# Kernel optimization log

Measured on AMD Instinct MI355X. Metric: run time of the kernel, lower is better.

## Reference

```python
import jax, jax.numpy as jnp
import numpy as np

NEG = -1e7  # matches replace_masked value -10000000.0


def tree_lstm(x, graph, wx, bx, uh, bh):
    # x: (B,T,I); graph: (B,T,T); wx: (4,H,I) gates [i,f,o,u]; uh: (4,H,H)
    B, T, _ = x.shape
    H = wx.shape[1]
    # precompute input projections for all gates/timesteps: (B,T,4,H)
    xg = jnp.einsum('bti,ghi->btgh', x, wx) + bx[None, None]
    h0 = jnp.zeros((B, T, H), x.dtype)

    def step(carry, j):
        h, c = carry
        h_j = h[:, j]  # still zeros at step j, as in the original code
        i = jax.nn.sigmoid(xg[:, j, 0] + h_j @ uh[0].T + bh[0])
        o = jax.nn.sigmoid(xg[:, j, 2] + h_j @ uh[2].T + bh[2])
        u = jnp.tanh(xg[:, j, 3] + h_j @ uh[3].T + bh[3])
        # forget gate against every node's hidden state: (B,T,H)
        f = jax.nn.sigmoid(xg[:, j, 1][:, None, :] + h @ uh[1].T + bh[1])
        # masked neighbor aggregation: bmm(mask, f*c) with mask row j
        c_j = i * u + jnp.einsum('bt,bth->bh', graph[:, j], f * c)
        h_j_new = o * jnp.tanh(c_j)
        return (h.at[:, j].set(h_j_new), c.at[:, j].set(c_j)), None

    (h, c), _ = jax.lax.scan(step, (h0, jnp.zeros_like(h0)), jnp.arange(T))
    return h, c


def masked_softmax(scores, key_mask):
    # scores: (B,Q,K); key_mask: (B,K)
    scores = jnp.where(key_mask[:, None, :] > 0, scores, NEG)
    return jax.nn.softmax(scores, axis=-1)


def pool(v, mask):
    avg = jnp.sum(v * mask[:, :, None], axis=1) / jnp.sum(mask, axis=1, keepdims=True)
    mx = jnp.max(jnp.where(mask[:, :, None] > 0, v, NEG), axis=1)
    return avg, mx


def esim_forward(premises, premises_lengths, hypotheses, hypotheses_lengths,
                 lgraph, rgraph, emb,
                 enc_wx, enc_bx, enc_uh, enc_bh,
                 comp_wx, comp_bx, comp_uh, comp_bh,
                 proj_w, proj_b, cls_w1, cls_b1, cls_w2, cls_b2):
    Tp = premises.shape[1]
    Th = hypotheses.shape[1]
    p_mask = (jnp.arange(Tp)[None, :] < premises_lengths[:, None]).astype(emb.dtype)
    h_mask = (jnp.arange(Th)[None, :] < hypotheses_lengths[:, None]).astype(emb.dtype)

    emb_p = emb[premises]
    emb_h = emb[hypotheses]

    enc_p, _ = tree_lstm(emb_p, lgraph, enc_wx, enc_bx, enc_uh, enc_bh)
    enc_h, _ = tree_lstm(emb_h, rgraph, enc_wx, enc_bx, enc_uh, enc_bh)

    # soft alignment attention
    sim = jnp.einsum('bph,bqh->bpq', enc_p, enc_h)
    att_p = masked_softmax(sim, h_mask) @ enc_h                      # (B,Tp,H)
    att_h = masked_softmax(sim.transpose(0, 2, 1), p_mask) @ enc_p   # (B,Th,H)

    enh_p = jnp.concatenate([enc_p, att_p, enc_p - att_p, enc_p * att_p], axis=-1)
    enh_h = jnp.concatenate([enc_h, att_h, enc_h - att_h, enc_h * att_h], axis=-1)

    proj_p = jax.nn.relu(enh_p @ proj_w.T + proj_b)
    proj_h = jax.nn.relu(enh_h @ proj_w.T + proj_b)

    v_ai, _ = tree_lstm(proj_p, lgraph, comp_wx, comp_bx, comp_uh, comp_bh)
    v_bj, _ = tree_lstm(proj_h, rgraph, comp_wx, comp_bx, comp_uh, comp_bh)

    a_avg, a_max = pool(v_ai, p_mask)
    b_avg, b_max = pool(v_bj, h_mask)
    v = jnp.concatenate([a_avg, a_max, b_avg, b_max], axis=1)

    hid = jnp.tanh(v @ cls_w1.T + cls_b1)
    logits = hid @ cls_w2.T + cls_b2
    return logits


def setup_inputs() -> dict:
    B, T, E, H, V, C = 32, 128, 300, 300, 50000, 3
    key = jax.random.key(0)
    ks = jax.random.split(key, 20)
    premises = jax.random.randint(ks[0], (B, T), 1, V)
    premises_lengths = jax.random.randint(ks[1], (B,), T // 2, T + 1)
    hypotheses = jax.random.randint(ks[2], (B, T), 1, V)
    hypotheses_lengths = jax.random.randint(ks[3], (B,), T // 2, T + 1)
    # sparse binary adjacency (~1-2 children per node), as in dependency trees
    lgraph = (jax.random.uniform(ks[4], (B, T, T)) < 0.01).astype(jnp.float32)
    rgraph = (jax.random.uniform(ks[5], (B, T, T)) < 0.01).astype(jnp.float32)
    emb = jax.random.normal(ks[6], (V, E), jnp.float32) * 0.05
    emb = emb.at[0].set(0.0)  # padding_idx=0

    def g(k, shape, fan_in):
        return jax.random.normal(k, shape, jnp.float32) * (1.0 / np.sqrt(fan_in))

    return {
        'premises': premises, 'premises_lengths': premises_lengths,
        'hypotheses': hypotheses, 'hypotheses_lengths': hypotheses_lengths,
        'lgraph': lgraph, 'rgraph': rgraph, 'emb': emb,
        'enc_wx': g(ks[7], (4, H, E), E), 'enc_bx': jnp.zeros((4, H), jnp.float32),
        'enc_uh': g(ks[8], (4, H, H), H), 'enc_bh': jnp.zeros((4, H), jnp.float32),
        'comp_wx': g(ks[9], (4, H, H), H), 'comp_bx': jnp.zeros((4, H), jnp.float32),
        'comp_uh': g(ks[10], (4, H, H), H), 'comp_bh': jnp.zeros((4, H), jnp.float32),
        'proj_w': g(ks[11], (H, 4 * H), 4 * H), 'proj_b': jnp.zeros((H,), jnp.float32),
        'cls_w1': g(ks[12], (H, 4 * H), 4 * H), 'cls_b1': jnp.zeros((H,), jnp.float32),
        'cls_w2': g(ks[13], (C, H), H), 'cls_b2': jnp.zeros((C,), jnp.float32),
    }


def reference(premises, premises_lengths, hypotheses, hypotheses_lengths,
              lgraph, rgraph, emb,
              enc_wx, enc_bx, enc_uh, enc_bh,
              comp_wx, comp_bx, comp_uh, comp_bh,
              proj_w, proj_b, cls_w1, cls_b1, cls_w2, cls_b2):
    return esim_forward(premises, premises_lengths, hypotheses, hypotheses_lengths,
                        lgraph, rgraph, emb,
                        enc_wx, enc_bx, enc_uh, enc_bh,
                        comp_wx, comp_bx, comp_uh, comp_bh,
                        proj_w, proj_b, cls_w1, cls_b1, cls_w2, cls_b2)
```

## Files before the change

kernel.cpp:

```cpp
#include <hip/hip_runtime.h>
#include <math.h>

#define B_ 32
#define T_ 128
#define H_ 300
#define HG 1200
#define LMAX 10
#define WLCAP 8192
#define ECAP 2048
#define NEGV -10000000.0f

typedef __attribute__((ext_vector_type(8))) short bf16x8;
typedef __attribute__((ext_vector_type(4))) float f32x4;
typedef unsigned short ushort_t;

__device__ __forceinline__ float sigm(float x){ return 1.f/(1.f+expf(-x)); }

__device__ __forceinline__ unsigned short f2bf(float x){
  union { float f; unsigned int u; } c; c.f = x;
  unsigned int u = c.u;
  return (unsigned short)((u + 0x7fffu + ((u >> 16) & 1u)) >> 16);
}
__device__ __forceinline__ float bf2f(unsigned short h){
  union { unsigned int u; float f; } c; c.u = ((unsigned int)h) << 16;
  return c.f;
}

__global__ __launch_bounds__(256) void k_prep_all(
    const float* __restrict__ enc_uh, const float* __restrict__ comp_uh,
    const float* __restrict__ enc_wx, const float* __restrict__ comp_wx,
    const float* __restrict__ pw, const float* __restrict__ cw1,
    float* __restrict__ te, float* __restrict__ tc, float* __restrict__ w1t,
    ushort_t* __restrict__ WencH, ushort_t* __restrict__ WencL,
    ushort_t* __restrict__ WcompH, ushort_t* __restrict__ WcompL,
    ushort_t* __restrict__ WPH, ushort_t* __restrict__ WPL)
{
  int i = blockIdx.x*256 + threadIdx.x;
  if (i < 90000) {
    int m = i / H_, k = i - m*H_;
    te[i] = enc_uh[H_*H_ + (size_t)k*H_ + m];
    tc[i] = comp_uh[H_*H_ + (size_t)k*H_ + m];
  } else if (i < 450000) {
    int i2 = i - 90000;
    int m = i2 / H_, k = i2 - m*H_;
    w1t[i2] = cw1[(size_t)k*HG + m];
  } else if (i < 834000) {
    int i2 = i - 450000;
    int n = i2 / 320, k = i2 - n*320;
    float v = (k < 300) ? enc_wx[(size_t)n*300 + k] : 0.f;
    ushort_t h = f2bf(v);
    WencH[i2] = h; WencL[i2] = f2bf(v - bf2f(h));
  } else if (i < 1218000) {
    int i2 = i - 834000;
    int n = i2 / 320, k = i2 - n*320;
    float v = (k < 300) ? comp_wx[(size_t)n*300 + k] : 0.f;
    ushort_t h = f2bf(v);
    WcompH[i2] = h; WcompL[i2] = f2bf(v - bf2f(h));
  } else if (i < 1496400) {
    int i2 = i - 1218000;
    int n = i2 / 928, k = i2 - n*928;
    const float* r = pw + (size_t)n*HG;
    float v = 0.f;
    if (k < 300)      v = r[k] + r[600+k];
    else if (k < 600) v = r[k] - r[k+300];
    else if (k < 900) v = r[k+300];
    ushort_t h = f2bf(v);
    WPH[i2] = h; WPL[i2] = f2bf(v - bf2f(h));
  }
}

__global__ __launch_bounds__(256) void k_embed_split(const int* __restrict__ prem, const int* __restrict__ hyp,
    const float* __restrict__ emb, ushort_t* __restrict__ EH, ushort_t* __restrict__ EL)
{
  int i = blockIdx.x*256 + threadIdx.x;
  int bt = i / 320, k = i - bt*320;
  int side = bt >> 12, bt2 = bt & 4095;
  float v = 0.f;
  if (k < 300) {
    int tok = (side == 0 ? prem : hyp)[bt2];
    v = emb[(size_t)tok*H_ + k];
  }
  ushort_t h = f2bf(v);
  EH[i] = h; EL[i] = f2bf(v - bf2f(h));
}

__global__ __launch_bounds__(256) void k_enh_split(const float* __restrict__ H1, const float* __restrict__ ATT,
    ushort_t* __restrict__ AH, ushort_t* __restrict__ AL)
{
  int i = blockIdx.x*256 + threadIdx.x;
  int r = i / 928, k = i - r*928;
  float v = 0.f;
  if (k < 300)      v = H1[(size_t)r*H_ + k];
  else if (k < 600) v = ATT[(size_t)r*H_ + k - 300];
  else if (k < 900) { int kk = k - 600; v = H1[(size_t)r*H_ + kk] * ATT[(size_t)r*H_ + kk]; }
  ushort_t h = f2bf(v);
  AH[i] = h; AL[i] = f2bf(v - bf2f(h));
}

__global__ __launch_bounds__(256) void k_build(const float* __restrict__ lg, const float* __restrict__ rg,
    int* __restrict__ cnt_g, int* __restrict__ coff_g, int* __restrict__ eidx_g, float* __restrict__ ew_g,
    int* __restrict__ hasp_g, int* __restrict__ depth_g, int* __restrict__ maxd_g,
    int* __restrict__ lvlcnt_g, int* __restrict__ wl_g)
{
  int chain = blockIdx.x; int s = chain >> 5, b = chain & 31;
  const float* graph = (s ? rg : lg) + (size_t)b*T_*T_;
  int tid = threadIdx.x;
  __shared__ float gbuf[T_*T_];
  __shared__ int cnt[T_], coff[T_], depth[T_], hasp[T_];
  __shared__ short eidx[ECAP];
  __shared__ float ew[ECAP];
  __shared__ int lcnt[LMAX], lbase[LMAX], lpos[LMAX];
  __shared__ int etot_s;

  #pragma unroll
  for (int k = 0; k < 16; ++k)
    ((float4*)gbuf)[tid + k*256] = ((const float4*)graph)[tid + k*256];
  if (tid < T_) hasp[tid] = 0;
  if (tid < LMAX) { lcnt[tid] = 0; lpos[tid] = 0; }
  __syncthreads();
  if (tid < T_) {
    int j = tid, c = 0;
    const float* gr = gbuf + j*T_;
    for (int t = 0; t < j; ++t) c += (gr[t] != 0.f) ? 1 : 0;
    cnt[j] = c;
  }
  __syncthreads();
  if (tid == 0) { int a = 0; for (int j = 0; j < T_; ++j) { coff[j] = a; a += cnt[j]; } etot_s = a; }
  __syncthreads();
  if (tid < T_) {
    int j = tid, p = coff[j];
    const float* gr = gbuf + j*T_;
    for (int t = 0; t < j; ++t) {
      float g = gr[t];
      if (g != 0.f && p < ECAP) { eidx[p] = (short)t; ew[p] = g; hasp[t] = 1; ++p; }
    }
  }
  __syncthreads();
  if (tid == 0) {
    int md = 0;
    for (int j = 0; j < T_; ++j) {
      int d = 0, e0 = coff[j], e1 = coff[j] + cnt[j];
      if (e1 > ECAP) e1 = ECAP;
      for (int k = e0; k < e1; ++k) { int dd = depth[eidx[k]] + 1; d = dd > d ? dd : d; }
      depth[j] = d; md = d > md ? d : md;
    }
    maxd_g[chain] = md;
  }
  __syncthreads();
  if (tid < T_) { int L = depth[tid]; if (L < LMAX) atomicAdd(&lcnt[L], 1); }
  __syncthreads();
  if (tid < LMAX && lcnt[tid] > 0) lbase[tid] = atomicAdd(&lvlcnt_g[tid], lcnt[tid]);
  __syncthreads();
  if (tid < T_) {
    int L = depth[tid];
    if (L < LMAX) {
      int p = atomicAdd(&lpos[L], 1);
      wl_g[L*WLCAP + lbase[L] + p] = (chain << 8) | tid;
    }
  }
  int base = chain * T_;
  if (tid < T_) {
    cnt_g[base+tid] = cnt[tid]; coff_g[base+tid] = coff[tid];
    hasp_g[base+tid] = hasp[tid]; depth_g[base+tid] = depth[tid];
  }
  int etot = etot_s; if (etot > ECAP) etot = ECAP;
  for (int i = tid; i < etot; i += 256) { eidx_g[chain*ECAP + i] = eidx[i]; ew_g[chain*ECAP + i] = ew[i]; }
}

__global__ __launch_bounds__(1024) void k_level(
    const float* __restrict__ xg, const float* __restrict__ bhv, const float* __restrict__ uh1T,
    const int* __restrict__ cnt_g, const int* __restrict__ coff_g,
    const int* __restrict__ eidx_g, const float* __restrict__ ew_g,
    const int* __restrict__ hasp_g, const int* __restrict__ lvlcnt_g, const int* __restrict__ wl_g,
    int L, float* __restrict__ hout, float* __restrict__ chist, float* __restrict__ fh)
{
  int count = lvlcnt_g[L];
  int nblk = (count + 3) >> 2;
  int tid = threadIdx.x;
  __shared__ float h_s[4][H_];
  __shared__ float psum[3][4][H_];
  __shared__ int nodes[4];
  __shared__ int anyp;
  for (int blk = blockIdx.x; blk < nblk; blk += gridDim.x) {
    int base = blk * 4;
    int nn = count - base; if (nn > 4) nn = 4;
    if (tid == 0) anyp = 0;
    __syncthreads();
    if (tid < 4) {
      int pk = (tid < nn) ? wl_g[L*WLCAP + base + tid] : -1;
      nodes[tid] = pk;
      if (pk >= 0 && hasp_g[(pk >> 8)*T_ + (pk & 255)]) atomicAdd(&anyp, 1);
    }
    __syncthreads();
    for (int w = tid; w < nn*H_; w += 1024) {
      int n = w / H_, e = w - n*H_;
      int pk = nodes[n]; int chain = pk >> 8, j = pk & 255;
      size_t cb = (size_t)chain*T_*H_, xb = (size_t)chain*T_*HG;
      const float* xp = xg + xb + (size_t)j*HG;
      float x0 = xp[e], x1 = xp[H_+e], x2 = xp[2*H_+e], x3 = xp[3*H_+e];
      float iu  = sigm(x0 + bhv[e]) * tanhf(x3 + bhv[3*H_+e]);
      float og  = sigm(x2 + bhv[2*H_+e]);
      float x1b = x1 + bhv[H_+e];
      float acc = iu;
      int c0 = coff_g[chain*T_+j], c1 = c0 + cnt_g[chain*T_+j];
      const int* ei = eidx_g + chain*ECAP;
      const float* ewp = ew_g + chain*ECAP;
      for (int k = c0; k < c1; ++k) {
        int t = ei[k];
        acc += ewp[k] * sigm(x1b + fh[cb + (size_t)t*H_ + e]) * chist[cb + (size_t)t*H_ + e];
      }
      chist[cb + (size_t)j*H_ + e] = acc;
      float hv = og * tanhf(acc);
      hout[cb + (size_t)j*H_ + e] = hv;
      h_s[n][e] = hv;
    }
    __syncthreads();
    if (anyp > 0) {
      if (tid < 3*H_) {
        int g = tid / H_, e = tid - g*H_;
        float a0=0.f, a1=0.f, a2=0.f, a3=0.f;
        const float* up = uh1T + e;
        int m0 = g*100, m1 = m0 + 100;
        #pragma unroll 4
        for (int m = m0; m < m1; ++m) {
          float u = up[(size_t)m*H_];
          a0 = fmaf(u, h_s[0][m], a0);
          a1 = fmaf(u, h_s[1][m], a1);
          a2 = fmaf(u, h_s[2][m], a2);
          a3 = fmaf(u, h_s[3][m], a3);
        }
        psum[g][0][e]=a0; psum[g][1][e]=a1; psum[g][2][e]=a2; psum[g][3][e]=a3;
      }
      __syncthreads();
      for (int w = tid; w < nn*H_; w += 1024) {
        int n = w / H_, e = w - n*H_;
        int pk = nodes[n]; int chain = pk >> 8, j = pk & 255;
        if (hasp_g[chain*T_+j]) {
          size_t cb = (size_t)chain*T_*H_;
          fh[cb + (size_t)j*H_ + e] = psum[0][n][e] + psum[1][n][e] + psum[2][n][e];
        }
      }
    }
    __syncthreads();
  }
}

__global__ __launch_bounds__(320) void k_tail(const float* __restrict__ xg, const float* __restrict__ bhv,
    const float* __restrict__ uh1T, const int* __restrict__ cnt_g, const int* __restrict__ coff_g,
    const int* __restrict__ eidx_g, const float* __restrict__ ew_g, const int* __restrict__ hasp_g,
    const int* __restrict__ depth_g, const int* __restrict__ maxd_g,
    float* __restrict__ hout, float* __restrict__ chist, float* __restrict__ fh)
{
  int chain = blockIdx.x;
  if (maxd_g[chain] < LMAX) return;
  int tid = threadIdx.x;
  bool act = tid < H_;
  float bh0=0.f,bh1=0.f,bh2=0.f,bh3=0.f;
  if (act) { bh0=bhv[tid]; bh1=bhv[H_+tid]; bh2=bhv[2*H_+tid]; bh3=bhv[3*H_+tid]; }
  __shared__ float h_lds[H_];
  size_t cb = (size_t)chain*T_*H_, xb = (size_t)chain*T_*HG;
  const int* ei = eidx_g + chain*ECAP;
  const float* ewp = ew_g + chain*ECAP;
  for (int j = 0; j < T_; ++j) {
    if (depth_g[chain*T_+j] < LMAX) continue;
    if (act) {
      const float* xp = xg + xb + (size_t)j*HG;
      float x0 = xp[tid], x1 = xp[H_+tid], x2 = xp[2*H_+tid], x3 = xp[3*H_+tid];
      float acc = sigm(x0+bh0) * tanhf(x3+bh3);
      float og  = sigm(x2+bh2);
      float x1b = x1 + bh1;
      int c0 = coff_g[chain*T_+j], c1 = c0 + cnt_g[chain*T_+j];
      for (int k = c0; k < c1; ++k) {
        int t = ei[k];
        acc += ewp[k] * sigm(x1b + fh[cb + (size_t)t*H_ + tid]) * chist[cb + (size_t)t*H_ + tid];
      }
      chist[cb + (size_t)j*H_ + tid] = acc;
      float hv = og * tanhf(acc);
      hout[cb + (size_t)j*H_ + tid] = hv;
      h_lds[tid] = hv;
    }
    __syncthreads();
    if (hasp_g[chain*T_+j] && act) {
      float a = 0.f;
      const float* up = uh1T + tid;
      #pragma unroll 4
      for (int m = 0; m < H_; ++m) a = fmaf(up[(size_t)m*H_], h_lds[m], a);
      fh[cb + (size_t)j*H_ + tid] = a;
    }
    __syncthreads();
  }
}

template<int OUTBF>
__global__ __launch_bounds__(256) void k_gemm_bf(
    const ushort_t* __restrict__ Ah, const ushort_t* __restrict__ Al, int AS,
    const ushort_t* __restrict__ Wh, const ushort_t* __restrict__ Wl, int WS,
    const float* __restrict__ bias, float* __restrict__ C,
    ushort_t* __restrict__ Ch, ushort_t* __restrict__ Cl, int CS,
    int N, int NT, int act)
{
  __shared__ ushort_t sAh[128*32], sAl[128*32], sWh[128*32], sWl[128*32];
  int tid = threadIdx.x;
  int bn = blockIdx.x * 128, bm = blockIdx.y * 128;
  int lane = tid & 63, wave = tid >> 6;
  int wr = (wave >> 1) * 64, wc = (wave & 1) * 64;
  int lrow = lane & 15, q = lane >> 4;

  int srow = tid >> 1, half = tid & 1;
  int ssw = (srow >> 1) & 3;
  int sg0 = ((2*half) ^ ssw) * 8, sg1 = ((2*half+1) ^ ssw) * 8;
  int sbase = srow * 32;
  const ushort_t* pAh = Ah + (size_t)(bm + srow)*AS + half*16;
  const ushort_t* pAl = Al + (size_t)(bm + srow)*AS + half*16;
  int wrow = bn + srow;
  int wsafe = (wrow < N) ? wrow : 0;
  const ushort_t* pWh = Wh + (size_t)wsafe*WS + half*16;
  const ushort_t* pWl = Wl + (size_t)wsafe*WS + half*16;

  bf16x8 rA0, rA1, rAl0, rAl1, rW0, rW1, rWl0, rWl1;
  auto issue = [&](int t){
    int kb = t * 32;
    rA0  = *(const bf16x8*)(pAh + kb); rA1  = *(const bf16x8*)(pAh + kb + 8);
    rAl0 = *(const bf16x8*)(pAl + kb); rAl1 = *(const bf16x8*)(pAl + kb + 8);
    rW0  = *(const bf16x8*)(pWh + kb); rW1  = *(const bf16x8*)(pWh + kb + 8);
    rWl0 = *(const bf16x8*)(pWl + kb); rWl1 = *(const bf16x8*)(pWl + kb + 8);
  };
  auto commit = [&](){
    *(bf16x8*)&sAh[sbase + sg0] = rA0; *(bf16x8*)&sAh[sbase + sg1] = rA1;
    *(bf16x8*)&sAl[sbase + sg0] = rAl0; *(bf16x8*)&sAl[sbase + sg1] = rAl1;
    *(bf16x8*)&sWh[sbase + sg0] = rW0; *(bf16x8*)&sWh[sbase + sg1] = rW1;
    *(bf16x8*)&sWl[sbase + sg0] = rWl0; *(bf16x8*)&sWl[sbase + sg1] = rWl1;
  };

  f32x4 acc[4][4];
  #pragma unroll
  for (int m = 0; m < 4; ++m)
    #pragma unroll
    for (int n = 0; n < 4; ++n) acc[m][n] = (f32x4){0.f,0.f,0.f,0.f};

  issue(0); commit();
  __syncthreads();
  for (int t = 0; t < NT; ++t) {
    bool more = (t+1 < NT);
    if (more) issue(t+1);
    bf16x8 ah[4], al[4], bh[4], bl[4];
    #pragma unroll
    for (int m = 0; m < 4; ++m) {
      int R = wr + m*16 + lrow;
      int o = R*32 + ((q ^ ((R>>1)&3)) * 8);
      ah[m] = *(const bf16x8*)&sAh[o];
      al[m] = *(const bf16x8*)&sAl[o];
    }
    #pragma unroll
    for (int n = 0; n < 4; ++n) {
      int R = wc + n*16 + lrow;
      int o = R*32 + ((q ^ ((R>>1)&3)) * 8);
      bh[n] = *(const bf16x8*)&sWh[o];
      bl[n] = *(const bf16x8*)&sWl[o];
    }
    #pragma unroll
    for (int m = 0; m < 4; ++m)
      #pragma unroll
      for (int n = 0; n < 4; ++n) {
        acc[m][n] = __builtin_amdgcn_mfma_f32_16x16x32_bf16(ah[m], bh[n], acc[m][n], 0,0,0);
        acc[m][n] = __builtin_amdgcn_mfma_f32_16x16x32_bf16(ah[m], bl[n], acc[m][n], 0,0,0);
        acc[m][n] = __builtin_amdgcn_mfma_f32_16x16x32_bf16(al[m], bh[n], acc[m][n], 0,0,0);
      }
    __syncthreads();
    if (more) commit();
    __syncthreads();
  }
  #pragma unroll
  for (int m = 0; m < 4; ++m) {
    int row0 = bm + wr + m*16 + (lane >> 4)*4;
    #pragma unroll
    for (int n = 0; n < 4; ++n) {
      int col = bn + wc + n*16 + lrow;
      if (OUTBF) {
        if (col < CS) {
          float bv = (col < N) ? bias[col] : 0.f;
          #pragma unroll
          for (int r = 0; r < 4; ++r) {
            float v = 0.f;
            if (col < N) { v = acc[m][n][r] + bv; if (act) v = fmaxf(v, 0.f); }
            ushort_t h = f2bf(v);
            Ch[(size_t)(row0 + r)*CS + col] = h;
            Cl[(size_t)(row0 + r)*CS + col] = f2bf(v - bf2f(h));
          }
        }
      } else {
        if (col < N) {
          float bv = bias[col];
          #pragma unroll
          for (int r = 0; r < 4; ++r) {
            float v = acc[m][n][r] + bv;
            if (act) v = fmaxf(v, 0.f);
            C[(size_t)(row0 + r)*N + col] = v;
          }
        }
      }
    }
  }
}

__global__ __launch_bounds__(256) void k_attn_mfma(
    const float* __restrict__ Hm, const int* __restrict__ plen, const int* __restrict__ hlen,
    float* __restrict__ ATT)
{
  __shared__ float regA_f[12800];
  __shared__ ushort_t pbuf[2*64*136];
  ushort_t* regA = (ushort_t*)regA_f;

  int tid = threadIdx.x;
  int lane = tid & 63, wave = tid >> 6;
  int lrow = lane & 15, koff = (lane >> 4) * 8;
  int d = blockIdx.x, b = blockIdx.y, q0 = blockIdx.z * 64;
  const float* Q  = Hm + ((size_t)(d*B_ + b)*T_ + q0) * H_;
  const float* Kp = Hm + ((size_t)((1-d)*B_ + b)*T_) * H_;
  float* outp = ATT + ((size_t)(d*B_ + b)*T_ + q0) * H_;
  int klen = (d == 0) ? hlen[b] : plen[b];

  ushort_t* sQh = regA;
  ushort_t* sQl = regA + 2560;
  ushort_t* sKh = regA + 5120;
  ushort_t* sKl = regA + 10240;
  int qrow = tid >> 2, qk0 = (tid & 3) * 8;
  int krow = tid >> 1, kk0 = (tid & 1) * 16;
  const float* Qr = Q + (size_t)qrow*H_;
  const float* Kr = Kp + (size_t)krow*H_;

  float4 gq[2], gk4[4];
  auto issue1 = [&](int t){
    int kb = t*32;
    #pragma unroll
    for (int i = 0; i < 2; ++i) {
      int g = kb + qk0 + i*4;
      gq[i] = make_float4(0.f,0.f,0.f,0.f);
      if (g < H_) gq[i] = *(const float4*)(Qr + g);
    }
    #pragma unroll
    for (int i = 0; i < 4; ++i) {
      int g = kb + kk0 + i*4;
      gk4[i] = make_float4(0.f,0.f,0.f,0.f);
      if (g < H_) gk4[i] = *(const float4*)(Kr + g);
    }
  };
  auto commit1 = [&](){
    #pragma unroll
    for (int i = 0; i < 2; ++i) {
      float4 v = gq[i]; ushort4 h, l;
      h.x=f2bf(v.x); h.y=f2bf(v.y); h.z=f2bf(v.z); h.w=f2bf(v.w);
      l.x=f2bf(v.x-bf2f(h.x)); l.y=f2bf(v.y-bf2f(h.y)); l.z=f2bf(v.z-bf2f(h.z)); l.w=f2bf(v.w-bf2f(h.w));
      int o = qrow*40 + qk0 + i*4;
      *(ushort4*)&sQh[o] = h; *(ushort4*)&sQl[o] = l;
    }
    #pragma unroll
    for (int i = 0; i < 4; ++i) {
      float4 v = gk4[i]; ushort4 h, l;
      h.x=f2bf(v.x); h.y=f2bf(v.y); h.z=f2bf(v.z); h.w=f2bf(v.w);
      l.x=f2bf(v.x-bf2f(h.x)); l.y=f2bf(v.y-bf2f(h.y)); l.z=f2bf(v.z-bf2f(h.z)); l.w=f2bf(v.w-bf2f(h.w));
      int o = krow*40 + kk0 + i*4;
      *(ushort4*)&sKh[o] = h; *(ushort4*)&sKl[o] = l;
    }
  };

  f32x4 acc1[4][2];
  #pragma unroll
  for (int m = 0; m < 4; ++m)
    #pragma unroll
    for (int n = 0; n < 2; ++n) acc1[m][n] = (f32x4){0.f,0.f,0.f,0.f};
  int wc = wave * 32;

  issue1(0); commit1();
  __syncthreads();
  for (int t = 0; t < 10; ++t) {
    bool more = (t < 9);
    bf16x8 ah[4], al[4], bh[2], bl[2];
    #pragma unroll
    for (int m = 0; m < 4; ++m) {
      int o = (m*16 + lrow)*40 + koff;
      ah[m] = *(const bf16x8*)&sQh[o];
      al[m] = *(const bf16x8*)&sQl[o];
    }
    #pragma unroll
    for (int n = 0; n < 2; ++n) {
      int o = (wc + n*16 + lrow)*40 + koff;
      bh[n] = *(const bf16x8*)&sKh[o];
      bl[n] = *(const bf16x8*)&sKl[o];
    }
    if (more) issue1(t+1);
    __syncthreads();
    if (more) commit1();
    #pragma unroll
    for (int m = 0; m < 4; ++m)
      #pragma unroll
      for (int n = 0; n < 2; ++n) {
        acc1[m][n] = __builtin_amdgcn_mfma_f32_16x16x32_bf16(ah[m], bh[n], acc1[m][n], 0,0,0);
        acc1[m][n] = __builtin_amdgcn_mfma_f32_16x16x32_bf16(ah[m], bl[n], acc1[m][n], 0,0,0);
        acc1[m][n] = __builtin_amdgcn_mfma_f32_16x16x32_bf16(al[m], bh[n], acc1[m][n], 0,0,0);
      }
    __syncthreads();
  }
  float* sim = regA_f;
  #pragma unroll
  for (int m = 0; m < 4; ++m)
    #pragma unroll
    for (int n = 0; n < 2; ++n)
      #pragma unroll
      for (int r = 0; r < 4; ++r)
        sim[(m*16 + (lane>>4)*4 + r)*132 + wc + n*16 + lrow] = acc1[m][n][r];
  __syncthreads();

  {
    int row = tid >> 2, qtr = (tid & 3) * 32;
    const float* sr = sim + row*132;
    float mx = NEGV;
    for (int c = 0; c < 32; ++c) { int cg = qtr + c; float s = (cg < klen) ? sr[cg] : NEGV; mx = fmaxf(mx, s); }
    mx = fmaxf(mx, __shfl_xor(mx, 1));
    mx = fmaxf(mx, __shfl_xor(mx, 2));
    float sum = 0.f;
    for (int c = 0; c < 32; ++c) { int cg = qtr + c; if (cg < klen) sum += expf(sr[cg] - mx); }
    sum += __shfl_xor(sum, 1);
    sum += __shfl_xor(sum, 2);
    float rinv = 1.f / sum;
    for (int c = 0; c < 32; ++c) {
      int cg = qtr + c;
      float p = (cg < klen) ? expf(sr[cg] - mx) * rinv : 0.f;
      ushort_t h = f2bf(p);
      pbuf[row*136 + cg] = h;
      pbuf[64*136 + row*136 + cg] = f2bf(p - bf2f(h));
    }
  }
  __syncthreads();

  ushort_t* kth = regA;
  ushort_t* ktl = regA + 12800;
  int wr2 = (wave & 1) * 32;
  int wcf = (wave >> 1) * 160;
  f32x4 acc3[2][10];
  #pragma unroll
  for (int m = 0; m < 2; ++m)
    #pragma unroll
    for (int n = 0; n < 10; ++n) acc3[m][n] = (f32x4){0.f,0.f,0.f,0.f};
  int skey = tid >> 3, sf4 = tid & 7;

  for (int kc = 0; kc < 4; ++kc) {
    __syncthreads();
    const float* kr = Kp + (size_t)(kc*32 + skey)*H_;
    for (int f4 = sf4; f4 < 75; f4 += 8) {
      float4 v = *(const float4*)(kr + f4*4);
      float vv[4] = {v.x, v.y, v.z, v.w};
      #pragma unroll
      for (int i = 0; i < 4; ++i) {
        int feat = f4*4 + i;
        ushort_t h = f2bf(vv[i]);
        kth[feat*40 + skey] = h;
        ktl[feat*40 + skey] = f2bf(vv[i] - bf2f(h));
      }
    }
    __syncthreads();
    bf16x8 ph[2], pl[2], kh[10], kl[10];
    #pragma unroll
    for (int m = 0; m < 2; ++m) {
      int o = (wr2 + m*16 + lrow)*136 + kc*32 + koff;
      ph[m] = *(const bf16x8*)&pbuf[o];
      pl[m] = *(const bf16x8*)&pbuf[64*136 + o];
    }
    #pragma unroll
    for (int n = 0; n < 10; ++n) {
      int o = (wcf + n*16 + lrow)*40 + koff;
      kh[n] = *(const bf16x8*)&kth[o];
      kl[n] = *(const bf16x8*)&ktl[o];
    }
    #pragma unroll
    for (int m = 0; m < 2; ++m)
      #pragma unroll
      for (int n = 0; n < 10; ++n) {
        acc3[m][n] = __builtin_amdgcn_mfma_f32_16x16x32_bf16(ph[m], kh[n], acc3[m][n], 0,0,0);
        acc3[m][n] = __builtin_amdgcn_mfma_f32_16x16x32_bf16(ph[m], kl[n], acc3[m][n], 0,0,0);
        acc3[m][n] = __builtin_amdgcn_mfma_f32_16x16x32_bf16(pl[m], kh[n], acc3[m][n], 0,0,0);
      }
  }
  #pragma unroll
  for (int m = 0; m < 2; ++m) {
    int row0 = wr2 + m*16 + (lane >> 4)*4;
    #pragma unroll
    for (int n = 0; n < 10; ++n) {
      int col = wcf + n*16 + lrow;
      if (col < H_) {
        #pragma unroll
        for (int r = 0; r < 4; ++r)
          outp[(size_t)(row0 + r)*H_ + col] = acc3[m][n][r];
      }
    }
  }
}

__global__ __launch_bounds__(320) void k_pool(const float* __restrict__ H,
    const int* __restrict__ plen, const int* __restrict__ hlen,
    float* __restrict__ psum, float* __restrict__ pmax)
{
  int chain = blockIdx.x; int s = chain >> 5, b = chain & 31;
  int c = blockIdx.y; int t0 = c * 16;
  int len = (s == 0 ? plen[b] : hlen[b]);
  int tid = threadIdx.x;
  __shared__ float buf[16*H_];
  const float* hp = H + (size_t)chain*T_*H_ + (size_t)t0*H_;
  for (int i = tid; i < 16*H_; i += 320) buf[i] = hp[i];
  __syncthreads();
  if (tid < H_) {
    int tmax = len - t0; if (tmax > 16) tmax = 16;
    float sum = 0.f, mx = NEGV;
    for (int t = 0; t < tmax; ++t) { float x = buf[t*H_ + tid]; sum += x; mx = fmaxf(mx, x); }
    int o = (chain*8 + c)*H_ + tid;
    psum[o] = sum; pmax[o] = mx;
  }
}

__global__ __launch_bounds__(320) void k_classify(
    const float* __restrict__ psum, const float* __restrict__ pmax,
    const int* __restrict__ plen, const int* __restrict__ hlen,
    const float* __restrict__ w1t, const float* __restrict__ b1,
    const float* __restrict__ w2, const float* __restrict__ b2,
    float* __restrict__ out)
{
  int b = blockIdx.x;
  int tid = threadIdx.x;
  __shared__ float v[HG];
  __shared__ float hid[H_];
  for (int s = 0; s < 2; ++s) {
    int chain = s*B_ + b;
    int len = (s == 0 ? plen[b] : hlen[b]);
    if (tid < H_) {
      float sum = 0.f, mx = NEGV;
      #pragma unroll
      for (int c = 0; c < 8; ++c) {
        int o = (chain*8 + c)*H_ + tid;
        sum += psum[o]; mx = fmaxf(mx, pmax[o]);
      }
      v[s*600 + tid]       = sum / (float)len;
      v[s*600 + 300 + tid] = mx;
    }
  }
  __syncthreads();
  if (tid < H_) {
    float a0 = b1[tid], a1 = 0.f, a2 = 0.f, a3 = 0.f;
    for (int m = 0; m < HG; m += 4) {
      a0 = fmaf(v[m+0], w1t[(size_t)(m+0)*H_ + tid], a0);
      a1 = fmaf(v[m+1], w1t[(size_t)(m+1)*H_ + tid], a1);
      a2 = fmaf(v[m+2], w1t[(size_t)(m+2)*H_ + tid], a2);
      a3 = fmaf(v[m+3], w1t[(size_t)(m+3)*H_ + tid], a3);
    }
    hid[tid] = tanhf(a0 + a1 + a2 + a3);
  }
  __syncthreads();
  if (tid < 3) {
    float a = b2[tid];
    const float* wr = w2 + (size_t)tid*H_;
    for (int n = 0; n < H_; ++n) a = fmaf(hid[n], wr[n], a);
    out[b*3 + tid] = a;
  }
}

extern "C" void kernel_launch(void* const* d_in, const int* in_sizes, int n_in,
                              void* d_out, int out_size, void* d_ws, size_t ws_size,
                              hipStream_t stream) {
  const int*   prem    = (const int*)d_in[0];
  const int*   plen    = (const int*)d_in[1];
  const int*   hyp     = (const int*)d_in[2];
  const int*   hlen    = (const int*)d_in[3];
  const float* lg      = (const float*)d_in[4];
  const float* rg      = (const float*)d_in[5];
  const float* emb     = (const float*)d_in[6];
  const float* enc_wx  = (const float*)d_in[7];
  const float* enc_bx  = (const float*)d_in[8];
  const float* enc_uh  = (const float*)d_in[9];
  const float* enc_bh  = (const float*)d_in[10];
  const float* comp_wx = (const float*)d_in[11];
  const float* comp_bx = (const float*)d_in[12];
  const float* comp_uh = (const float*)d_in[13];
  const float* comp_bh = (const float*)d_in[14];
  const float* proj_w  = (const float*)d_in[15];
  const float* proj_b  = (const float*)d_in[16];
  const float* cls_w1  = (const float*)d_in[17];
  const float* cls_b1  = (const float*)d_in[18];
  const float* cls_w2  = (const float*)d_in[19];
  const float* cls_b2  = (const float*)d_in[20];
  float* outp = (float*)d_out;

  float* XG  = (float*)d_ws;
  ushort_t* EH = (ushort_t*)(XG + 9830400);
  ushort_t* EL = EH + 2621440;
  float* H1  = XG + 9830400 + 2621440;
  float* CH  = H1 + 2457600;
  float* FH  = CH + 2457600;
  float* UTE = FH + 2457600;
  float* UTC = UTE + 90000;
  float* W1T = UTC + 90000;
  ushort_t* WencH  = (ushort_t*)(W1T + 360000);
  ushort_t* WencL  = WencH + 384000;
  ushort_t* WcompH = WencL + 384000;
  ushort_t* WcompL = WcompH + 384000;
  ushort_t* WPH    = WcompL + 384000;
  ushort_t* WPL    = WPH + 278400;
  float* PSUM = W1T + 360000 + 1046400;
  float* PMAX = PSUM + 153600;
  float* EW   = PMAX + 153600;
  int* EIDX   = (int*)(EW + 64*ECAP);
  int* CNT    = EIDX + 64*ECAP;
  int* COFF   = CNT + 64*T_;
  int* DEPTH  = COFF + 64*T_;
  int* HASP   = DEPTH + 64*T_;
  int* MAXD   = HASP + 64*T_;
  int* LVLCNT = MAXD + 64;
  int* WL     = LVLCNT + LMAX;
  float* ATT  = CH;
  ushort_t* ENH_H = (ushort_t*)XG;
  ushort_t* ENH_L = ENH_H + 7602176;

  hipMemsetAsync(LVLCNT, 0, LMAX*sizeof(int), stream);
  k_prep_all<<<(1496400 + 255)/256, 256, 0, stream>>>(enc_uh, comp_uh, enc_wx, comp_wx, proj_w, cls_w1,
      UTE, UTC, W1T, WencH, WencL, WcompH, WcompL, WPH, WPL);
  k_build<<<64, 256, 0, stream>>>(lg, rg, CNT, COFF, EIDX, EW, HASP, DEPTH, MAXD, LVLCNT, WL);
  k_embed_split<<<10240, 256, 0, stream>>>(prem, hyp, emb, EH, EL);
  k_gemm_bf<0><<<dim3(10, 64), 256, 0, stream>>>(EH, EL, 320, WencH, WencL, 320,
      enc_bx, XG, nullptr, nullptr, 0, HG, 10, 0);
  for (int L = 0; L < LMAX; ++L)
    k_level<<<640, 1024, 0, stream>>>(XG, enc_bh, UTE, CNT, COFF, EIDX, EW, HASP, LVLCNT, WL, L, H1, CH, FH);
  k_tail<<<64, 320, 0, stream>>>(XG, enc_bh, UTE, CNT, COFF, EIDX, EW, HASP, DEPTH, MAXD, H1, CH, FH);
  k_attn_mfma<<<dim3(2, B_, 2), 256, 0, stream>>>(H1, plen, hlen, ATT);
  k_enh_split<<<29696, 256, 0, stream>>>(H1, ATT, ENH_H, ENH_L);
  k_gemm_bf<1><<<dim3(3, 64), 256, 0, stream>>>(ENH_H, ENH_L, 928, WPH, WPL, 928,
      proj_b, nullptr, EH, EL, 320, H_, 29, 1);
  k_gemm_bf<0><<<dim3(10, 64), 256, 0, stream>>>(EH, EL, 320, WcompH, WcompL, 320,
      comp_bx, XG, nullptr, nullptr, 0, HG, 10, 0);
  for (int L = 0; L < LMAX; ++L)
    k_level<<<640, 1024, 0, stream>>>(XG, comp_bh, UTC, CNT, COFF, EIDX, EW, HASP, LVLCNT, WL, L, H1, CH, FH);
  k_tail<<<64, 320, 0, stream>>>(XG, comp_bh, UTC, CNT, COFF, EIDX, EW, HASP, DEPTH, MAXD, H1, CH, FH);
  k_pool<<<dim3(64, 8), 320, 0, stream>>>(H1, plen, hlen, PSUM, PMAX);
  k_classify<<<B_, 320, 0, stream>>>(PSUM, PMAX, plen, hlen, W1T, cls_b1, cls_w2, cls_b2, outp);
}
```

Before: 520.0 us.

## Split first three tree levels into elementwise gate kernel and MFMA forget-gate GEMM

For the three shallowest tree levels, the fused per-level kernel is replaced by two kernels. An elementwise kernel computes the gates and cell/hidden states per node. A split-bf16 MFMA GEMM then computes h·U_f^T for all nodes in the level at once and writes them into the forget-gate buffer for later levels. Bf16 hi/lo copies of the forget recurrent weights are added to the prep kernel. The aim is to move the large, wide levels onto matrix cores instead of the per-block scalar matvec, at the cost of extra launches and three-term bf16 split precision.

```diff
diff --git a/kernel.cpp b/kernel.cpp
--- a/kernel.cpp
+++ b/kernel.cpp
@@ -33,7 +33,9 @@
     float* __restrict__ te, float* __restrict__ tc, float* __restrict__ w1t,
     ushort_t* __restrict__ WencH, ushort_t* __restrict__ WencL,
     ushort_t* __restrict__ WcompH, ushort_t* __restrict__ WcompL,
-    ushort_t* __restrict__ WPH, ushort_t* __restrict__ WPL)
+    ushort_t* __restrict__ WPH, ushort_t* __restrict__ WPL,
+    ushort_t* __restrict__ U1eH, ushort_t* __restrict__ U1eL,
+    ushort_t* __restrict__ U1cH, ushort_t* __restrict__ U1cL)
 {
   int i = blockIdx.x*256 + threadIdx.x;
   if (i < 90000) {
@@ -66,6 +68,18 @@
     else if (k < 900) v = r[k+300];
     ushort_t h = f2bf(v);
     WPH[i2] = h; WPL[i2] = f2bf(v - bf2f(h));
+  } else if (i < 1592400) {
+    int i2 = i - 1496400;
+    int n = i2 / 320, k = i2 - n*320;
+    float v = (k < 300) ? enc_uh[H_*H_ + (size_t)n*H_ + k] : 0.f;
+    ushort_t h = f2bf(v);
+    U1eH[i2] = h; U1eL[i2] = f2bf(v - bf2f(h));
+  } else if (i < 1688400) {
+    int i2 = i - 1592400;
+    int n = i2 / 320, k = i2 - n*320;
+    float v = (k < 300) ? comp_uh[H_*H_ + (size_t)n*H_ + k] : 0.f;
+    ushort_t h = f2bf(v);
+    U1cH[i2] = h; U1cL[i2] = f2bf(v - bf2f(h));
   }
 }
 
@@ -165,6 +179,153 @@
   }
   int etot = etot_s; if (etot > ECAP) etot = ECAP;
   for (int i = tid; i < etot; i += 256) { eidx_g[chain*ECAP + i] = eidx[i]; ew_g[chain*ECAP + i] = ew[i]; }
+}
+
+__global__ __launch_bounds__(256) void k_gates_level(
+    const float* __restrict__ xg, const float* __restrict__ bhv,
+    const int* __restrict__ cnt_g, const int* __restrict__ coff_g,
+    const int* __restrict__ eidx_g, const float* __restrict__ ew_g,
+    const int* __restrict__ lvlcnt_g, const int* __restrict__ wl_g, int L,
+    float* __restrict__ hout, float* __restrict__ chist, const float* __restrict__ fh)
+{
+  int count = lvlcnt_g[L];
+  int total = count * H_;
+  for (int idx = blockIdx.x*256 + threadIdx.x; idx < total; idx += gridDim.x*256) {
+    int n = idx / H_, e = idx - n*H_;
+    int pk = wl_g[L*WLCAP + n]; int chain = pk >> 8, j = pk & 255;
+    size_t cb = (size_t)chain*T_*H_, xb = (size_t)chain*T_*HG;
+    const float* xp = xg + xb + (size_t)j*HG;
+    float x0 = xp[e], x1 = xp[H_+e], x2 = xp[2*H_+e], x3 = xp[3*H_+e];
+    float iu  = sigm(x0 + bhv[e]) * tanhf(x3 + bhv[3*H_+e]);
+    float og  = sigm(x2 + bhv[2*H_+e]);
+    float x1b = x1 + bhv[H_+e];
+    float acc = iu;
+    int c0 = coff_g[chain*T_+j], c1 = c0 + cnt_g[chain*T_+j];
+    const int* ei = eidx_g + chain*ECAP;
+    const float* ewp = ew_g + chain*ECAP;
+    for (int k = c0; k < c1; ++k) {
+      int t = ei[k];
+      acc += ewp[k] * sigm(x1b + fh[cb + (size_t)t*H_ + e]) * chist[cb + (size_t)t*H_ + e];
+    }
+    chist[cb + (size_t)j*H_ + e] = acc;
+    hout[cb + (size_t)j*H_ + e] = og * tanhf(acc);
+  }
+}
+
+__global__ __launch_bounds__(256) void k_fh_gemm(
+    const float* __restrict__ Hin, const ushort_t* __restrict__ Uh, const ushort_t* __restrict__ Ul,
+    const int* __restrict__ lvlcnt_g, const int* __restrict__ wl_g, int L,
+    float* __restrict__ fhout)
+{
+  int count = lvlcnt_g[L];
+  int bm = blockIdx.y * 128;
+  if (bm >= count) return;
+  __shared__ ushort_t sAh[128*32], sAl[128*32], sWh[128*32], sWl[128*32];
+  int tid = threadIdx.x;
+  int bn = blockIdx.x * 128;
+  int lane = tid & 63, wave = tid >> 6;
+  int wr = (wave >> 1) * 64, wc = (wave & 1) * 64;
+  int lrow = lane & 15, q = lane >> 4;
+
+  int srow = tid >> 1, half = tid & 1;
+  int ssw = (srow >> 1) & 3;
+  int sg0 = ((2*half) ^ ssw) * 8, sg1 = ((2*half+1) ^ ssw) * 8;
+  int sbase = srow * 32;
+  int slot = bm + srow; if (slot >= count) slot = count - 1;
+  int pk = wl_g[L*WLCAP + slot];
+  const float* ApBase = Hin + (size_t)((pk >> 8)*T_ + (pk & 255)) * H_;
+  int brow = bn + srow;
+  int wsafe = (brow < H_) ? brow : 0;
+  const ushort_t* pWh = Uh + (size_t)wsafe*320 + half*16;
+  const ushort_t* pWl = Ul + (size_t)wsafe*320 + half*16;
+
+  float4 ga[4];
+  bf16x8 rW0, rW1, rWl0, rWl1;
+  auto issue = [&](int t){
+    int kb = t*32 + half*16;
+    #pragma unroll
+    for (int i = 0; i < 4; ++i) {
+      int gk = kb + i*4;
+      ga[i] = (gk < H_) ? *(const float4*)(ApBase + gk) : make_float4(0.f,0.f,0.f,0.f);
+    }
+    rW0  = *(const bf16x8*)(pWh + t*32);
+    rW1  = *(const bf16x8*)(pWh + t*32 + 8);
+    rWl0 = *(const bf16x8*)(pWl + t*32);
+    rWl1 = *(const bf16x8*)(pWl + t*32 + 8);
+  };
+  auto commit = [&](){
+    ushort_t h8[16], l8[16];
+    #pragma unroll
+    for (int i = 0; i < 4; ++i) {
+      float vv[4] = {ga[i].x, ga[i].y, ga[i].z, ga[i].w};
+      #pragma unroll
+      for (int u = 0; u < 4; ++u) {
+        ushort_t hh = f2bf(vv[u]);
+        h8[i*4+u] = hh; l8[i*4+u] = f2bf(vv[u] - bf2f(hh));
+      }
+    }
+    *(bf16x8*)&sAh[sbase+sg0] = *(bf16x8*)&h8[0]; *(bf16x8*)&sAh[sbase+sg1] = *(bf16x8*)&h8[8];
+    *(bf16x8*)&sAl[sbase+sg0] = *(bf16x8*)&l8[0]; *(bf16x8*)&sAl[sbase+sg1] = *(bf16x8*)&l8[8];
+    *(bf16x8*)&sWh[sbase+sg0] = rW0; *(bf16x8*)&sWh[sbase+sg1] = rW1;
+    *(bf16x8*)&sWl[sbase+sg0] = rWl0; *(bf16x8*)&sWl[sbase+sg1] = rWl1;
+  };
+
+  f32x4 acc[4][4];
+  #pragma unroll
+  for (int m = 0; m < 4; ++m)
+    #pragma unroll
+    for (int n = 0; n < 4; ++n) acc[m][n] = (f32x4){0.f,0.f,0.f,0.f};
+
+  issue(0); commit();
+  __syncthreads();
+  for (int t = 0; t < 10; ++t) {
+    bool more = (t+1 < 10);
+    if (more) issue(t+1);
+    bf16x8 ah[4], al[4], bh[4], bl[4];
+    #pragma unroll
+    for (int m = 0; m < 4; ++m) {
+      int R = wr + m*16 + lrow;
+      int o = R*32 + ((q ^ ((R>>1)&3)) * 8);
+      ah[m] = *(const bf16x8*)&sAh[o];
+      al[m] = *(const bf16x8*)&sAl[o];
+    }
+    #pragma unroll
+    for (int n = 0; n < 4; ++n) {
+      int R = wc + n*16 + lrow;
+      int o = R*32 + ((q ^ ((R>>1)&3)) * 8);
+      bh[n] = *(const bf16x8*)&sWh[o];
+      bl[n] = *(const bf16x8*)&sWl[o];
+    }
+    #pragma unroll
+    for (int m = 0; m < 4; ++m)
+      #pragma unroll
+      for (int n = 0; n < 4; ++n) {
+        acc[m][n] = __builtin_amdgcn_mfma_f32_16x16x32_bf16(ah[m], bh[n], acc[m][n], 0,0,0);
+        acc[m][n] = __builtin_amdgcn_mfma_f32_16x16x32_bf16(ah[m], bl[n], acc[m][n], 0,0,0);
+        acc[m][n] = __builtin_amdgcn_mfma_f32_16x16x32_bf16(al[m], bh[n], acc[m][n], 0,0,0);
+      }
+    __syncthreads();
+    if (more) commit();
+    __syncthreads();
+  }
+  #pragma unroll
+  for (int m = 0; m < 4; ++m) {
+    int tr0 = wr + m*16 + (lane >> 4)*4;
+    #pragma unroll
+    for (int n = 0; n < 4; ++n) {
+      int col = bn + wc + n*16 + lrow;
+      if (col < H_) {
+        #pragma unroll
+        for (int r = 0; r < 4; ++r) {
+          int slot2 = bm + tr0 + r;
+          if (slot2 < count) {
+            int pk2 = wl_g[L*WLCAP + slot2];
+            fhout[(size_t)((pk2>>8)*T_ + (pk2&255))*H_ + col] = acc[m][n][r];
+          }
+        }
+      }
+    }
+  }
 }
 
 __global__ __launch_bounds__(1024) void k_level(
@@ -703,7 +864,11 @@
   ushort_t* WcompL = WcompH + 384000;
   ushort_t* WPH    = WcompL + 384000;
   ushort_t* WPL    = WPH + 278400;
-  float* PSUM = W1T + 360000 + 1046400;
+  ushort_t* U1eH   = WPL + 278400;
+  ushort_t* U1eL   = U1eH + 96000;
+  ushort_t* U1cH   = U1eL + 96000;
+  ushort_t* U1cL   = U1cH + 96000;
+  float* PSUM = W1T + 360000 + 1046400 + 192000;
   float* PMAX = PSUM + 153600;
   float* EW   = PMAX + 153600;
   int* EIDX   = (int*)(EW + 64*ECAP);
@@ -719,13 +884,17 @@
   ushort_t* ENH_L = ENH_H + 7602176;
 
   hipMemsetAsync(LVLCNT, 0, LMAX*sizeof(int), stream);
-  k_prep_all<<<(1496400 + 255)/256, 256, 0, stream>>>(enc_uh, comp_uh, enc_wx, comp_wx, proj_w, cls_w1,
-      UTE, UTC, W1T, WencH, WencL, WcompH, WcompL, WPH, WPL);
+  k_prep_all<<<(1688400 + 255)/256, 256, 0, stream>>>(enc_uh, comp_uh, enc_wx, comp_wx, proj_w, cls_w1,
+      UTE, UTC, W1T, WencH, WencL, WcompH, WcompL, WPH, WPL, U1eH, U1eL, U1cH, U1cL);
   k_build<<<64, 256, 0, stream>>>(lg, rg, CNT, COFF, EIDX, EW, HASP, DEPTH, MAXD, LVLCNT, WL);
   k_embed_split<<<10240, 256, 0, stream>>>(prem, hyp, emb, EH, EL);
   k_gemm_bf<0><<<dim3(10, 64), 256, 0, stream>>>(EH, EL, 320, WencH, WencL, 320,
       enc_bx, XG, nullptr, nullptr, 0, HG, 10, 0);
-  for (int L = 0; L < LMAX; ++L)
+  for (int L = 0; L < 3; ++L) {
+    k_gates_level<<<2048, 256, 0, stream>>>(XG, enc_bh, CNT, COFF, EIDX, EW, LVLCNT, WL, L, H1, CH, FH);
+    k_fh_gemm<<<dim3(3, 64), 256, 0, stream>>>(H1, U1eH, U1eL, LVLCNT, WL, L, FH);
+  }
+  for (int L = 3; L < LMAX; ++L)
     k_level<<<640, 1024, 0, stream>>>(XG, enc_bh, UTE, CNT, COFF, EIDX, EW, HASP, LVLCNT, WL, L, H1, CH, FH);
   k_tail<<<64, 320, 0, stream>>>(XG, enc_bh, UTE, CNT, COFF, EIDX, EW, HASP, DEPTH, MAXD, H1, CH, FH);
   k_attn_mfma<<<dim3(2, B_, 2), 256, 0, stream>>>(H1, plen, hlen, ATT);
@@ -734,7 +903,11 @@
       proj_b, nullptr, EH, EL, 320, H_, 29, 1);
   k_gemm_bf<0><<<dim3(10, 64), 256, 0, stream>>>(EH, EL, 320, WcompH, WcompL, 320,
       comp_bx, XG, nullptr, nullptr, 0, HG, 10, 0);
-  for (int L = 0; L < LMAX; ++L)
+  for (int L = 0; L < 3; ++L) {
+    k_gates_level<<<2048, 256, 0, stream>>>(XG, comp_bh, CNT, COFF, EIDX, EW, LVLCNT, WL, L, H1, CH, FH);
+    k_fh_gemm<<<dim3(3, 64), 256, 0, stream>>>(H1, U1cH, U1cL, LVLCNT, WL, L, FH);
+  }
+  for (int L = 3; L < LMAX; ++L)
     k_level<<<640, 1024, 0, stream>>>(XG, comp_bh, UTC, CNT, COFF, EIDX, EW, HASP, LVLCNT, WL, L, H1, CH, FH);
   k_tail<<<64, 320, 0, stream>>>(XG, comp_bh, UTC, CNT, COFF, EIDX, EW, HASP, DEPTH, MAXD, H1, CH, FH);
   k_pool<<<dim3(64, 8), 320, 0, stream>>>(H1, plen, hlen, PSUM, PMAX);
```

Result: slower. 585.3 us (+12.6%).
